# Kernel tuning notes

Hardware: AMD Instinct MI355X
Metric: run time of the kernel (lower is better)

Reference implementation:

```python
import jax, jax.numpy as jnp
import numpy as np

CUTOFF = 5.0
BOX = 15.0
SPECIES = [1, 6, 8]
N_NODES = 10000
N_EDGES = 200000
ETAS = [0.01, 0.05, 0.1]
ZETAS = [1.0, 2.0, 4.0, 8.0]
LAMBDAS = [-1.0, 1.0]


def _cartesian_params():
    # matches torch.cartesian_prod(etas, zetas, lambdas): etas outermost
    e, zt, lb = np.meshgrid(np.float32(ETAS), np.float32(ZETAS), np.float32(LAMBDAS), indexing='ij')
    return e.ravel(), zt.ravel(), lb.ravel()  # each [24]


def _build_triplets(rng):
    # edges: edge_index[0]=j (source), edge_index[1]=i (target)
    j = rng.integers(0, N_NODES, N_EDGES)
    i = rng.integers(0, N_NODES, N_EDGES)
    edge_shift = rng.integers(-1, 2, (N_EDGES, 3)).astype(np.float32)
    # CSR of adj_t (row=i, col=j): for edge e, triplet partners k are cols of row j[e]
    order = np.argsort(i, kind='stable')
    cols = j[order]
    cnt = np.bincount(i, minlength=N_NODES)
    rowptr = np.concatenate([[0], np.cumsum(cnt)])
    num_trip = cnt[j]
    T = int(num_trip.sum())
    e_of_t = np.repeat(np.arange(N_EDGES), num_trip)
    starts = np.repeat(np.cumsum(num_trip) - num_trip, num_trip)
    local = np.arange(T) - starts
    idx_k = cols[rowptr[j[e_of_t]] + local]
    idx_i = i[e_of_t]
    idx_j = j[e_of_t]
    shift_t = edge_shift[e_of_t]
    m = idx_i != idx_k
    return idx_i[m], idx_j[m], idx_k[m], shift_t[m]


def setup_inputs() -> dict:
    rng = np.random.default_rng(0)
    pos = rng.uniform(0.0, BOX, (N_NODES, 3)).astype(np.float32)
    cell = (np.eye(3, dtype=np.float32) * BOX)[None]  # [1,3,3]
    z = np.asarray(SPECIES, dtype=np.int64)[rng.integers(0, 3, N_NODES)]
    batch = np.zeros(N_NODES, dtype=np.int64)
    idx_i, idx_j, idx_k, edge_shift_i = _build_triplets(rng)
    etas, zetas, lambdas = _cartesian_params()
    return {
        'pos': jnp.asarray(pos), 'cell': jnp.asarray(cell),
        'z': jnp.asarray(z), 'batch': jnp.asarray(batch),
        'idx_i': jnp.asarray(idx_i), 'idx_j': jnp.asarray(idx_j), 'idx_k': jnp.asarray(idx_k),
        'edge_shift_i': jnp.asarray(edge_shift_i),
        'etas': jnp.asarray(etas), 'zetas': jnp.asarray(zetas), 'lambdas': jnp.asarray(lambdas),
    }


def _cutoff_fn(r):
    return 0.5 * (jnp.cos(jnp.pi * r / CUTOFF) + 1.0) * (r < CUTOFF).astype(r.dtype)


def reference(pos, cell, z, batch, idx_i, idx_j, idx_k, edge_shift_i, etas, zetas, lambdas):
    n_nodes = pos.shape[0]
    pos_i = pos[idx_i]                       # [T,3]
    cell_t = cell[batch[idx_i]]              # [T,3,3]
    shift = jnp.einsum('ni,nij->nj', edge_shift_i, cell_t)
    vec_ij = pos[idx_j] - pos_i + shift
    vec_ik = pos[idx_k] - pos_i + shift
    r_ij = jnp.linalg.norm(vec_ij, axis=-1)
    r_ik = jnp.linalg.norm(vec_ik, axis=-1)
    r_jk = jnp.linalg.norm(vec_ik - vec_ij, axis=-1)
    cos_ijk = jnp.sum(vec_ij * vec_ik, axis=-1) / (r_ij * r_ik + 1e-12)

    # [P,T] angular descriptor; base (1 + lambda*cos) >= 0 since lambda = +/-1
    G4 = (jnp.power(2.0, 1.0 - zetas)[:, None]
          * jnp.power(1.0 + lambdas[:, None] * cos_ijk[None, :], zetas[:, None])
          * jnp.exp(-etas[:, None] * (r_ij**2 + r_ik**2 + r_jk**2)[None, :] / CUTOFF**2)
          * (_cutoff_fn(r_ij) * _cutoff_fn(r_ik) * _cutoff_fn(r_jk))[None, :])

    zj = z[idx_j]
    zk = z[idx_k]
    outs = []
    for sp in SPECIES:
        mask = ((zj == sp) & (zk == sp)).astype(G4.dtype)
        outs.append(jax.ops.segment_sum((G4 * mask).T, idx_i, num_segments=n_nodes).T / 2)
    pairs = [(SPECIES[a], SPECIES[b]) for a in range(len(SPECIES)) for b in range(a + 1, len(SPECIES))]
    for sp_j, sp_k in pairs:
        mask = (((zj == sp_j) & (zk == sp_k)) | ((zj == sp_k) & (zk == sp_j))).astype(G4.dtype)
        outs.append(jax.ops.segment_sum((G4 * mask).T, idx_i, num_segments=n_nodes).T / 2)
    return jnp.concatenate(outs, axis=0)  # [6*P, N]
```

## Files before the change

### kernel.cpp

```cpp
#include <hip/hip_runtime.h>
#include <math.h>

#define CUTOFF_R  5.0f
#define CUT2      25.0f
#define INV_CUT2  (1.0f / 25.0f)
#define PI_OVER_CUT (3.14159265358979323846f / CUTOFF_R)
#define NPARAM 24
#define TPT 4

__device__ __noinline__ void rare_accumulate(
    int i, int j, int k,
    float vjx, float vjy, float vjz,
    float vkx, float vky, float vkz,
    float r2ij, float r2ik, float r2jk,
    const int* __restrict__ z,
    const float* __restrict__ etas,
    float* __restrict__ out, int N)
{
    float rij = sqrtf(r2ij);
    float rik = sqrtf(r2ik);
    float rjk = sqrtf(r2jk);

    float fc = 0.125f * (cosf(PI_OVER_CUT * rij) + 1.0f)
                      * (cosf(PI_OVER_CUT * rik) + 1.0f)
                      * (cosf(PI_OVER_CUT * rjk) + 1.0f);

    float cos_ijk = (vjx * vkx + vjy * vky + vjz * vkz) / (rij * rik + 1e-12f);
    float ssum = (r2ij + r2ik + r2jk) * INV_CUT2;

    int zj = z[j], zk = z[k];
    int a = (zj == 1) ? 0 : ((zj == 6) ? 1 : 2);
    int c = (zk == 1) ? 0 : ((zk == 6) ? 1 : 2);
    int ch = (a == c) ? a : (2 + a + c);

    float* obase = out + (size_t)ch * NPARAM * N + i;
    float fch = 0.5f * fc;

    float bm = 1.0f - cos_ijk;
    float bp = 1.0f + cos_ijk;
    float pw[4][2];
    pw[0][0] = bm;                 pw[0][1] = bp;
    pw[1][0] = bm * bm;            pw[1][1] = bp * bp;
    pw[2][0] = pw[1][0]*pw[1][0];  pw[2][1] = pw[1][1]*pw[1][1];
    pw[3][0] = pw[2][0]*pw[2][0];  pw[3][1] = pw[2][1]*pw[2][1];
    const float coef[4] = {1.0f, 0.5f, 0.125f, 0.0078125f};

    #pragma unroll
    for (int e = 0; e < 3; ++e) {
        float ee = expf(-etas[e * 8] * ssum) * fch;
        #pragma unroll
        for (int zi = 0; zi < 4; ++zi) {
            float cz = coef[zi] * ee;
            atomicAdd(obase + (size_t)(e * 8 + zi * 2 + 0) * N, cz * pw[zi][0]);
            atomicAdd(obase + (size_t)(e * 8 + zi * 2 + 1) * N, cz * pw[zi][1]);
        }
    }
}

__global__ void pad_pos_kernel(const float* __restrict__ pos,
                               float4* __restrict__ pos4, int N)
{
    int u = blockIdx.x * blockDim.x + threadIdx.x;
    if (u < N)
        pos4[u] = make_float4(pos[3*u], pos[3*u+1], pos[3*u+2], 0.0f);
}

__global__ __launch_bounds__(256) void g4_kernel(
    const float4* __restrict__ pos4,
    const float* __restrict__ cell,
    const int*   __restrict__ z,
    const int*   __restrict__ idx_i,
    const int*   __restrict__ idx_j,
    const int*   __restrict__ idx_k,
    const float* __restrict__ shift,
    const float* __restrict__ etas,
    float* __restrict__ out,
    int T, int N)
{
    float C00 = cell[0], C01 = cell[1], C02 = cell[2];
    float C10 = cell[3], C11 = cell[4], C12 = cell[5];
    float C20 = cell[6], C21 = cell[7], C22 = cell[8];

    int tid  = blockIdx.x * blockDim.x + threadIdx.x;
    int base = tid * TPT;
    if (base >= T) return;

    int ii[TPT], jj[TPT], kk[TPT];
    float ss[3 * TPT];
    bool full = (base + TPT <= T);

    if (full) {
        int4 vi = *reinterpret_cast<const int4*>(idx_i + base);
        int4 vj = *reinterpret_cast<const int4*>(idx_j + base);
        int4 vk = *reinterpret_cast<const int4*>(idx_k + base);
        ii[0]=vi.x; ii[1]=vi.y; ii[2]=vi.z; ii[3]=vi.w;
        jj[0]=vj.x; jj[1]=vj.y; jj[2]=vj.z; jj[3]=vj.w;
        kk[0]=vk.x; kk[1]=vk.y; kk[2]=vk.z; kk[3]=vk.w;
        const float4* sp = reinterpret_cast<const float4*>(shift + 3 * base);
        float4 a = sp[0], b = sp[1], c = sp[2];
        ss[0]=a.x; ss[1]=a.y; ss[2]=a.z;  ss[3]=a.w;
        ss[4]=b.x; ss[5]=b.y; ss[6]=b.z;  ss[7]=b.w;
        ss[8]=c.x; ss[9]=c.y; ss[10]=c.z; ss[11]=c.w;
    } else {
        #pragma unroll
        for (int m = 0; m < TPT; ++m) {
            int t = base + m;
            int tc = (t < T) ? t : (T - 1);
            ii[m] = idx_i[tc]; jj[m] = idx_j[tc]; kk[m] = idx_k[tc];
            ss[3*m] = shift[3*tc]; ss[3*m+1] = shift[3*tc+1]; ss[3*m+2] = shift[3*tc+2];
        }
    }

    float4 pi_[TPT], pj_[TPT], pk_[TPT];
    #pragma unroll
    for (int m = 0; m < TPT; ++m) {
        pi_[m] = pos4[ii[m]];
        pj_[m] = pos4[jj[m]];
        pk_[m] = pos4[kk[m]];
    }

    float vjv[TPT][3], vkv[TPT][3], r2a[TPT][3];
    unsigned mask = 0;
    #pragma unroll
    for (int m = 0; m < TPT; ++m) {
        float s0 = ss[3*m], s1 = ss[3*m+1], s2 = ss[3*m+2];
        float shx = s0 * C00 + s1 * C10 + s2 * C20;
        float shy = s0 * C01 + s1 * C11 + s2 * C21;
        float shz = s0 * C02 + s1 * C12 + s2 * C22;

        float vjx = pj_[m].x - pi_[m].x + shx;
        float vjy = pj_[m].y - pi_[m].y + shy;
        float vjz = pj_[m].z - pi_[m].z + shz;
        float vkx = pk_[m].x - pi_[m].x + shx;
        float vky = pk_[m].y - pi_[m].y + shy;
        float vkz = pk_[m].z - pi_[m].z + shz;

        float r2ij = vjx*vjx + vjy*vjy + vjz*vjz;
        float r2ik = vkx*vkx + vky*vky + vkz*vkz;
        float dx = vkx - vjx, dy = vky - vjy, dz = vkz - vjz;
        float r2jk = dx*dx + dy*dy + dz*dz;

        vjv[m][0]=vjx; vjv[m][1]=vjy; vjv[m][2]=vjz;
        vkv[m][0]=vkx; vkv[m][1]=vky; vkv[m][2]=vkz;
        r2a[m][0]=r2ij; r2a[m][1]=r2ik; r2a[m][2]=r2jk;

        bool p = (r2ij < CUT2) & (r2ik < CUT2) & (r2jk < CUT2)
               & (full | (base + m < T));
        mask |= ((unsigned)p) << m;
    }

    if (mask) {
        #pragma unroll
        for (int m = 0; m < TPT; ++m) {
            if (mask & (1u << m)) {
                rare_accumulate(ii[m], jj[m], kk[m],
                                vjv[m][0], vjv[m][1], vjv[m][2],
                                vkv[m][0], vkv[m][1], vkv[m][2],
                                r2a[m][0], r2a[m][1], r2a[m][2],
                                z, etas, out, N);
            }
        }
    }
}

extern "C" void kernel_launch(void* const* d_in, const int* in_sizes, int n_in,
                              void* d_out, int out_size, void* d_ws, size_t ws_size,
                              hipStream_t stream) {
    const float* pos     = (const float*)d_in[0];
    const float* cell    = (const float*)d_in[1];
    const int*   z       = (const int*)d_in[2];
    const int*   idx_i   = (const int*)d_in[4];
    const int*   idx_j   = (const int*)d_in[5];
    const int*   idx_k   = (const int*)d_in[6];
    const float* shift   = (const float*)d_in[7];
    const float* etas    = (const float*)d_in[8];
    float* out = (float*)d_out;

    int T = in_sizes[4];
    int N = in_sizes[0] / 3;

    float4* pos4 = (float4*)d_ws;

    hipMemsetAsync(d_out, 0, (size_t)out_size * sizeof(float), stream);
    pad_pos_kernel<<<(N + 255) / 256, 256, 0, stream>>>(pos, pos4, N);

    int block = 256;
    long long threads_needed = ((long long)T + TPT - 1) / TPT;
    int grid = (int)((threads_needed + block - 1) / block);
    g4_kernel<<<grid, block, 0, stream>>>(pos4, cell, z,
                                          idx_i, idx_j, idx_k, shift,
                                          etas, out, T, N);
}
```

Measured before the change: 159.3 us.

## Exploit per-edge triplet runs to skip k loads when the ij pair is out of cutoff

Each thread now handles 16 consecutive triplets instead of 4. Triplets sharing the same (i,j) edge are contiguous, so the thread loads pos_i, pos_j and the shift once per run. It also computes r_ij, the ij cutoff factor and the j species class once per run. k positions are fetched only when r_ij is inside the cutoff, which avoids most random gathers since few edges pass. The larger per-thread chunk lowers parallelism and serialises the k gathers, losing their memory-level parallelism.

```diff
diff --git a/kernel.cpp b/kernel.cpp
--- a/kernel.cpp
+++ b/kernel.cpp
@@ -6,34 +6,32 @@
 #define INV_CUT2  (1.0f / 25.0f)
 #define PI_OVER_CUT (3.14159265358979323846f / CUTOFF_R)
 #define NPARAM 24
-#define TPT 4
+#define TPT 16
 
 __device__ __noinline__ void rare_accumulate(
-    int i, int j, int k,
+    int oi, int acls, int k,
     float vjx, float vjy, float vjz,
     float vkx, float vky, float vkz,
+    float rij, float fcij,
     float r2ij, float r2ik, float r2jk,
     const int* __restrict__ z,
     const float* __restrict__ etas,
     float* __restrict__ out, int N)
 {
-    float rij = sqrtf(r2ij);
     float rik = sqrtf(r2ik);
     float rjk = sqrtf(r2jk);
 
-    float fc = 0.125f * (cosf(PI_OVER_CUT * rij) + 1.0f)
-                      * (cosf(PI_OVER_CUT * rik) + 1.0f)
-                      * (cosf(PI_OVER_CUT * rjk) + 1.0f);
+    float fc = fcij * 0.25f * (cosf(PI_OVER_CUT * rik) + 1.0f)
+                            * (cosf(PI_OVER_CUT * rjk) + 1.0f);
 
     float cos_ijk = (vjx * vkx + vjy * vky + vjz * vkz) / (rij * rik + 1e-12f);
     float ssum = (r2ij + r2ik + r2jk) * INV_CUT2;
 
-    int zj = z[j], zk = z[k];
-    int a = (zj == 1) ? 0 : ((zj == 6) ? 1 : 2);
+    int zk = z[k];
     int c = (zk == 1) ? 0 : ((zk == 6) ? 1 : 2);
-    int ch = (a == c) ? a : (2 + a + c);
+    int ch = (acls == c) ? acls : (2 + acls + c);
 
-    float* obase = out + (size_t)ch * NPARAM * N + i;
+    float* obase = out + (size_t)ch * NPARAM * N + oi;
     float fch = 0.5f * fc;
 
     float bm = 1.0f - cos_ijk;
@@ -86,77 +84,77 @@
     if (base >= T) return;
 
     int ii[TPT], jj[TPT], kk[TPT];
-    float ss[3 * TPT];
     bool full = (base + TPT <= T);
 
     if (full) {
-        int4 vi = *reinterpret_cast<const int4*>(idx_i + base);
-        int4 vj = *reinterpret_cast<const int4*>(idx_j + base);
-        int4 vk = *reinterpret_cast<const int4*>(idx_k + base);
-        ii[0]=vi.x; ii[1]=vi.y; ii[2]=vi.z; ii[3]=vi.w;
-        jj[0]=vj.x; jj[1]=vj.y; jj[2]=vj.z; jj[3]=vj.w;
-        kk[0]=vk.x; kk[1]=vk.y; kk[2]=vk.z; kk[3]=vk.w;
-        const float4* sp = reinterpret_cast<const float4*>(shift + 3 * base);
-        float4 a = sp[0], b = sp[1], c = sp[2];
-        ss[0]=a.x; ss[1]=a.y; ss[2]=a.z;  ss[3]=a.w;
-        ss[4]=b.x; ss[5]=b.y; ss[6]=b.z;  ss[7]=b.w;
-        ss[8]=c.x; ss[9]=c.y; ss[10]=c.z; ss[11]=c.w;
+        #pragma unroll
+        for (int q = 0; q < TPT / 4; ++q) {
+            int4 a = *reinterpret_cast<const int4*>(idx_i + base + 4 * q);
+            int4 b = *reinterpret_cast<const int4*>(idx_j + base + 4 * q);
+            int4 c = *reinterpret_cast<const int4*>(idx_k + base + 4 * q);
+            ii[4*q+0]=a.x; ii[4*q+1]=a.y; ii[4*q+2]=a.z; ii[4*q+3]=a.w;
+            jj[4*q+0]=b.x; jj[4*q+1]=b.y; jj[4*q+2]=b.z; jj[4*q+3]=b.w;
+            kk[4*q+0]=c.x; kk[4*q+1]=c.y; kk[4*q+2]=c.z; kk[4*q+3]=c.w;
+        }
     } else {
         #pragma unroll
         for (int m = 0; m < TPT; ++m) {
             int t = base + m;
             int tc = (t < T) ? t : (T - 1);
             ii[m] = idx_i[tc]; jj[m] = idx_j[tc]; kk[m] = idx_k[tc];
-            ss[3*m] = shift[3*tc]; ss[3*m+1] = shift[3*tc+1]; ss[3*m+2] = shift[3*tc+2];
         }
     }
 
-    float4 pi_[TPT], pj_[TPT], pk_[TPT];
+    bool  alive = false;
+    int   cur_i = -1, cur_j = -1;
+    float ox = 0.f, oy = 0.f, oz = 0.f;
+    float vjx = 0.f, vjy = 0.f, vjz = 0.f;
+    float r2ij = 0.f, rij = 0.f, fcij = 0.f;
+    int   oi = 0, acls = 0;
+
     #pragma unroll
     for (int m = 0; m < TPT; ++m) {
-        pi_[m] = pos4[ii[m]];
-        pj_[m] = pos4[jj[m]];
-        pk_[m] = pos4[kk[m]];
-    }
+        int t  = base + m;
+        int tc = (t < T) ? t : (T - 1);
+        int i = ii[m], j = jj[m];
 
-    float vjv[TPT][3], vkv[TPT][3], r2a[TPT][3];
-    unsigned mask = 0;
-    #pragma unroll
-    for (int m = 0; m < TPT; ++m) {
-        float s0 = ss[3*m], s1 = ss[3*m+1], s2 = ss[3*m+2];
-        float shx = s0 * C00 + s1 * C10 + s2 * C20;
-        float shy = s0 * C01 + s1 * C11 + s2 * C21;
-        float shz = s0 * C02 + s1 * C12 + s2 * C22;
+        bool newrun = (m == 0) | (i != cur_i) | (j != cur_j);
+        if (newrun) {
+            cur_i = i; cur_j = j;
+            float s0 = shift[3*tc+0], s1 = shift[3*tc+1], s2 = shift[3*tc+2];
+            float shx = s0 * C00 + s1 * C10 + s2 * C20;
+            float shy = s0 * C01 + s1 * C11 + s2 * C21;
+            float shz = s0 * C02 + s1 * C12 + s2 * C22;
 
-        float vjx = pj_[m].x - pi_[m].x + shx;
-        float vjy = pj_[m].y - pi_[m].y + shy;
-        float vjz = pj_[m].z - pi_[m].z + shz;
-        float vkx = pk_[m].x - pi_[m].x + shx;
-        float vky = pk_[m].y - pi_[m].y + shy;
-        float vkz = pk_[m].z - pi_[m].z + shz;
+            float4 pi = pos4[i];
+            float4 pj = pos4[j];
+            ox = shx - pi.x; oy = shy - pi.y; oz = shz - pi.z;
+            vjx = pj.x + ox; vjy = pj.y + oy; vjz = pj.z + oz;
+            r2ij = vjx*vjx + vjy*vjy + vjz*vjz;
+            alive = (r2ij < CUT2);
+            if (alive) {
+                rij  = sqrtf(r2ij);
+                fcij = 0.5f * (cosf(PI_OVER_CUT * rij) + 1.0f);
+                oi   = i;
+                int zj = z[j];
+                acls = (zj == 1) ? 0 : ((zj == 6) ? 1 : 2);
+            }
+        }
 
-        float r2ij = vjx*vjx + vjy*vjy + vjz*vjz;
-        float r2ik = vkx*vkx + vky*vky + vkz*vkz;
-        float dx = vkx - vjx, dy = vky - vjy, dz = vkz - vjz;
-        float r2jk = dx*dx + dy*dy + dz*dz;
-
-        vjv[m][0]=vjx; vjv[m][1]=vjy; vjv[m][2]=vjz;
-        vkv[m][0]=vkx; vkv[m][1]=vky; vkv[m][2]=vkz;
-        r2a[m][0]=r2ij; r2a[m][1]=r2ik; r2a[m][2]=r2jk;
-
-        bool p = (r2ij < CUT2) & (r2ik < CUT2) & (r2jk < CUT2)
-               & (full | (base + m < T));
-        mask |= ((unsigned)p) << m;
-    }
-
-    if (mask) {
-        #pragma unroll
-        for (int m = 0; m < TPT; ++m) {
-            if (mask & (1u << m)) {
-                rare_accumulate(ii[m], jj[m], kk[m],
-                                vjv[m][0], vjv[m][1], vjv[m][2],
-                                vkv[m][0], vkv[m][1], vkv[m][2],
-                                r2a[m][0], r2a[m][1], r2a[m][2],
+        bool valid = alive & (t < T);
+        if (valid) {
+            int k = kk[m];
+            float4 pk = pos4[k];
+            float vkx = pk.x + ox;
+            float vky = pk.y + oy;
+            float vkz = pk.z + oz;
+            float r2ik = vkx*vkx + vky*vky + vkz*vkz;
+            float dx = vkx - vjx, dy = vky - vjy, dz = vkz - vjz;
+            float r2jk = dx*dx + dy*dy + dz*dz;
+            if ((r2ik < CUT2) & (r2jk < CUT2)) {
+                rare_accumulate(oi, acls, k,
+                                vjx, vjy, vjz, vkx, vky, vkz,
+                                rij, fcij, r2ij, r2ik, r2jk,
                                 z, etas, out, N);
             }
         }
```

After: 171.7 us. +7.8%, slower.
